# Kernel tuning notes

Hardware: AMD Instinct MI355X
Metric: run time of the kernel (lower is better)

Reference implementation:

```python
import jax, jax.numpy as jnp
import numpy as np

N = 50000          # nodes
E = 800000         # edges (avg degree 16)
NFEAT = 128        # dim_touched / gcn_nfeat
NHID = 96
NCLASS = 64
EXTRA = 32         # extra MLP-only features
NHID1, NHID2 = 128, 64
NN = 70            # top-k threshold rank
EPS = 1e-5         # BatchNorm1d eps


def setup_inputs() -> dict:
    key = jax.random.key(0)
    ks = jax.random.split(key, 24)
    x = jax.random.normal(ks[0], (N, NFEAT + EXTRA + 1), jnp.float32)
    grp = jax.random.randint(ks[1], (N,), 0, 2).astype(jnp.float32)
    x = x.at[:, -1].set(grp)  # last column is the group flag (target_group == 0)
    row = jax.random.randint(ks[2], (E,), 0, N, dtype=jnp.int32)
    col = jax.random.randint(ks[3], (E,), 0, N, dtype=jnp.int32)
    val = jax.random.uniform(ks[4], (E,), jnp.float32)

    def p(k, shape):
        return (jax.random.normal(k, shape, jnp.float32) * 0.05)

    return dict(
        x=x, row=row, col=col, val=val,
        W1=p(ks[5], (NFEAT, NHID)), b1=p(ks[6], (NHID,)),
        W2=p(ks[7], (NHID, NHID)), b2=p(ks[8], (NHID,)),
        W3=p(ks[9], (NHID, NHID)), b3=p(ks[10], (NHID,)),
        W4=p(ks[11], (NHID, NHID)), b4=p(ks[12], (NHID,)),
        W5=p(ks[13], (NHID, NCLASS)), b5=p(ks[14], (NCLASS,)),
        M1w=p(ks[15], (NCLASS + EXTRA, NHID1)), M1b=p(ks[16], (NHID1,)),
        M2w=p(ks[17], (NHID1, NHID2)), M2b=p(ks[18], (NHID2,)),
        M3w=p(ks[19], (NHID2, 1)), M3b=p(ks[20], (1,)),
    )


def _bn(h):
    # fresh BatchNorm1d in training mode, affine at default init (gamma=1, beta=0)
    m = jnp.mean(h, axis=0)
    v = jnp.mean((h - m) ** 2, axis=0)  # biased variance, as used for normalization
    return (h - m) * jax.lax.rsqrt(v + EPS)


def _gc(h, row, col, val, W, b):
    # GraphConvolution: spmm(adj, h @ W) + b, adj in COO form
    s = h @ W                                            # [N, out]
    msg = val[:, None] * s[col]                          # [E, out]
    agg = jax.ops.segment_sum(msg, row, num_segments=N)  # [N, out]
    return agg + b


def reference(x, row, col, val, W1, b1, W2, b2, W3, b3, W4, b4, W5, b5,
              M1w, M1b, M2w, M2b, M3w, M3b):
    h = x[:, :NFEAT]
    h = _bn(jax.nn.relu(_gc(h, row, col, val, W1, b1)))
    h = _bn(jax.nn.relu(_gc(h, row, col, val, W2, b2)))
    h = _bn(jax.nn.relu(_gc(h, row, col, val, W3, b3)))
    h = _bn(jax.nn.relu(_gc(h, row, col, val, W4, b4)))
    h = jax.nn.relu(_gc(h, row, col, val, W5, b5))        # [N, NCLASS]

    feat = jnp.concatenate([h, x[:, NFEAT:-1]], axis=1)   # [N, NCLASS+EXTRA]
    m = jax.nn.relu(feat @ M1w + M1b)
    m = jax.nn.relu(m @ M2w + M2b)
    m = m @ M3w + M3b                                     # [N, 1]

    # mask out target_group rows with the global min
    m = jnp.where(x[:, -1:] == 0.0, jnp.min(m), m)        # [N, 1]

    # top-70 threshold: value at descending rank NN
    thresh = jax.lax.top_k(m[:, 0], NN + 1)[0][NN]
    recip = jax.lax.stop_gradient(1.0 / m)                # torch reciprocal on detach()
    mask = jnp.where(m > thresh, recip, jnp.zeros_like(m))
    return m * mask
```

## Files before the change

kernel.cpp:

```cpp
#include <hip/hip_runtime.h>
#include <cstdint>
#include <cstddef>

#define XLD 161
#define GA  2048

typedef float f4u __attribute__((ext_vector_type(4), aligned(4)));
typedef float f4a __attribute__((ext_vector_type(4)));
typedef float f3u __attribute__((ext_vector_type(3), aligned(4)));
typedef float f2a __attribute__((ext_vector_type(2)));

__global__ void hist_kernel(const int* __restrict__ row, int* __restrict__ cnt, int E) {
    for (int e = blockIdx.x * blockDim.x + threadIdx.x; e < E; e += gridDim.x * blockDim.x)
        atomicAdd(&cnt[row[e]], 1);
}

__global__ __launch_bounds__(256)
void scan1_kernel(const int* __restrict__ cnt, int* __restrict__ offs,
                  int* __restrict__ bsums, int n) {
    int t = threadIdx.x;
    int gid = blockIdx.x * 256 + t;
    int v = (gid < n) ? cnt[gid] : 0;
    int x = v;
#pragma unroll
    for (int o = 1; o < 64; o <<= 1) { int y = __shfl_up(x, o); if ((t & 63) >= o) x += y; }
    __shared__ int ws[4];
    if ((t & 63) == 63) ws[t >> 6] = x;
    __syncthreads();
    int add = 0;
    for (int w = 0; w < (t >> 6); w++) add += ws[w];
    int incl = x + add;
    if (gid < n) offs[gid] = incl - v;
    if (t == 255) bsums[blockIdx.x] = incl;
}

__global__ __launch_bounds__(256)
void scan2_kernel(int* __restrict__ bsums, int nb) {
    int t = threadIdx.x;
    int v = (t < nb) ? bsums[t] : 0;
    int x = v;
#pragma unroll
    for (int o = 1; o < 64; o <<= 1) { int y = __shfl_up(x, o); if ((t & 63) >= o) x += y; }
    __shared__ int ws[4];
    if ((t & 63) == 63) ws[t >> 6] = x;
    __syncthreads();
    int add = 0;
    for (int w = 0; w < (t >> 6); w++) add += ws[w];
    if (t < nb) bsums[t] = x + add - v;
}

__global__ void scan3_kernel(int* __restrict__ offs, int* __restrict__ cursor,
                             const int* __restrict__ bsums, int n, int E) {
    int gid = blockIdx.x * 256 + threadIdx.x;
    if (gid < n) {
        int o = offs[gid] + bsums[blockIdx.x];
        offs[gid] = o;
        cursor[gid] = o;
    }
    if (gid == 0) offs[n] = E;
}

__global__ void scatter_kernel(const int* __restrict__ row, const int* __restrict__ col,
                               const float* __restrict__ val, int* __restrict__ cursor,
                               int2* __restrict__ cvA, int E) {
    for (int e = blockIdx.x * blockDim.x + threadIdx.x; e < E; e += gridDim.x * blockDim.x) {
        int r = row[e];
        int p = atomicAdd(&cursor[r], 1);
        cvA[p] = make_int2(col[e], __float_as_int(val[e]));
    }
}

template <int LC, bool WVS>
__global__ __launch_bounds__(256)
void aggP(const float* __restrict__ S, int ldS, const int* __restrict__ offs,
          const int2* __restrict__ cvA,
          float* __restrict__ Aout, float* __restrict__ vout, int n) {
    int lane = threadIdx.x & 63;
    int lg   = lane & 31;
    int grp  = threadIdx.x >> 5;
    int sh   = lane & 32;

    for (int node = blockIdx.x * 8 + grp; node < n; node += gridDim.x * 8) {
        int e0 = offs[node], e1 = offs[node + 1];
        float acc[LC];
#pragma unroll
        for (int a = 0; a < LC; a++) acc[a] = 0.f;
        float vsum = 0.f;

        for (int e = e0; e < e1; e += 32) {
            int   idx = e + lg;
            int2  cv = (idx < e1) ? cvA[idx] : make_int2(0, 0);
            int   ce = cv.x;
            float ve = __int_as_float(cv.y);
            int   cnt = min(32, e1 - e);
#pragma unroll 8
            for (int j = 0; j < cnt; j++) {
                int   c = __shfl(ce, sh + j);
                float v = __shfl(ve, sh + j);
                const float* srow = S + (size_t)c * ldS + LC * lg;
                if (LC == 3) {
                    f3u g = *(const f3u*)srow;
                    acc[0] = fmaf(v, g[0], acc[0]);
                    acc[1] = fmaf(v, g[1], acc[1]);
                    acc[2] = fmaf(v, g[2], acc[2]);
                } else {
                    f4u g = *(const f4u*)srow;
                    acc[0] = fmaf(v, g[0], acc[0]);
                    acc[1] = fmaf(v, g[1], acc[1]);
                    acc[2] = fmaf(v, g[2], acc[2]);
                    acc[3] = fmaf(v, g[3], acc[3]);
                }
                vsum += v;
            }
        }

        float* orow = Aout + (size_t)node * (32 * LC) + LC * lg;
        if (LC == 3) {
            f3u o; o[0] = acc[0]; o[1] = acc[1]; o[2] = acc[2];
            *(f3u*)orow = o;
        } else {
            f4u o; o[0] = acc[0]; o[1] = acc[1]; o[2] = acc[2]; o[3] = acc[3];
            *(f4u*)orow = o;
        }
        if (WVS && lg == 0) vout[node] = vsum;
    }
}

__global__ __launch_bounds__(256)
void aggB(const float* __restrict__ S, const int* __restrict__ offs,
          const int2* __restrict__ cvA, const float* __restrict__ bias,
          float* __restrict__ Hout, float* __restrict__ vout,
          float* __restrict__ pbuf, int n) {
    __shared__ float sS[96], sQ[96];
    int t = threadIdx.x;
    if (t < 96) { sS[t] = 0.f; sQ[t] = 0.f; }
    __syncthreads();
    int lane = t & 63, lg = lane & 31, grp = t >> 5, sh = lane & 32;
    float bb[3];
    bb[0] = bias[3 * lg]; bb[1] = bias[3 * lg + 1]; bb[2] = bias[3 * lg + 2];
    float ps[3] = {0.f, 0.f, 0.f}, pq[3] = {0.f, 0.f, 0.f};

    for (int node = blockIdx.x * 8 + grp; node < n; node += gridDim.x * 8) {
        int e0 = offs[node], e1 = offs[node + 1];
        float acc[3] = {0.f, 0.f, 0.f};
        float vsum = 0.f;
        for (int e = e0; e < e1; e += 32) {
            int   idx = e + lg;
            int2  cv = (idx < e1) ? cvA[idx] : make_int2(0, 0);
            int   ce = cv.x;
            float ve = __int_as_float(cv.y);
            int   cnt = min(32, e1 - e);
#pragma unroll 8
            for (int j = 0; j < cnt; j++) {
                int   c = __shfl(ce, sh + j);
                float v = __shfl(ve, sh + j);
                const float* srow = S + (size_t)c * 96 + 3 * lg;
                f3u g = *(const f3u*)srow;
                acc[0] = fmaf(v, g[0], acc[0]);
                acc[1] = fmaf(v, g[1], acc[1]);
                acc[2] = fmaf(v, g[2], acc[2]);
                vsum += v;
            }
        }
        float* orow = Hout + (size_t)node * 96 + 3 * lg;
        f3u o;
#pragma unroll
        for (int a = 0; a < 3; a++) {
            float v = fmaxf(acc[a] + bb[a], 0.f);
            o[a] = v;
            ps[a] += v; pq[a] += v * v;
        }
        *(f3u*)orow = o;
        if (lg == 0) vout[node] = vsum;
    }
#pragma unroll
    for (int a = 0; a < 3; a++) {
        atomicAdd(&sS[3 * lg + a], ps[a]);
        atomicAdd(&sQ[3 * lg + a], pq[a]);
    }
    __syncthreads();
    if (t < 96) {
        pbuf[(size_t)blockIdx.x * 192 + t]      = sS[t];
        pbuf[(size_t)blockIdx.x * 192 + 96 + t] = sQ[t];
    }
}

__global__ __launch_bounds__(256)
void bn_reduce(const float* __restrict__ pbuf, float* __restrict__ stats, int nb) {
    int t = threadIdx.x;
    if (t < 192) {
        float s = 0.f;
        for (int pb = blockIdx.x; pb < nb; pb += gridDim.x)
            s += pbuf[(size_t)pb * 192 + t];
        atomicAdd(&stats[t], s);
    }
}

__global__ __launch_bounds__(256)
void aggC(const float* __restrict__ S, const int* __restrict__ offs,
          const int2* __restrict__ cvA, const float* __restrict__ bias,
          const float* __restrict__ cb, const float* __restrict__ vsum,
          float* __restrict__ Hout, int n) {
    int lane = threadIdx.x & 63, lg = lane & 31, grp = threadIdx.x >> 5, sh = lane & 32;
    float bb0 = bias[2 * lg], bb1 = bias[2 * lg + 1];
    float cc0 = cb[2 * lg],   cc1 = cb[2 * lg + 1];

    for (int node = blockIdx.x * 8 + grp; node < n; node += gridDim.x * 8) {
        int e0 = offs[node], e1 = offs[node + 1];
        float a0 = 0.f, a1 = 0.f;
        for (int e = e0; e < e1; e += 32) {
            int   idx = e + lg;
            int2  cv = (idx < e1) ? cvA[idx] : make_int2(0, 0);
            int   ce = cv.x;
            float ve = __int_as_float(cv.y);
            int   cnt = min(32, e1 - e);
#pragma unroll 8
            for (int j = 0; j < cnt; j++) {
                int   c = __shfl(ce, sh + j);
                float v = __shfl(ve, sh + j);
                f2a g = *(const f2a*)(S + (size_t)c * 64 + 2 * lg);
                a0 = fmaf(v, g[0], a0);
                a1 = fmaf(v, g[1], a1);
            }
        }
        float vs = vsum[node];
        f2a o;
        o[0] = fmaxf(a0 + vs * cc0 + bb0, 0.f);
        o[1] = fmaxf(a1 + vs * cc1 + bb1, 0.f);
        *(f2a*)(Hout + (size_t)node * 64 + 2 * lg) = o;
    }
}

template <int CT>
__device__ inline void ldw(const float* p, float* wv) {
    if constexpr (CT == 4) { *(f4a*)wv = *(const f4a*)p; }
    else if constexpr (CT == 6) { *(f3u*)wv = *(const f3u*)p; *(f3u*)(wv + 3) = *(const f3u*)(p + 3); }
    else { *(f4a*)wv = *(const f4a*)p; *(f4a*)(wv + 4) = *(const f4a*)(p + 4); }
}

template <int K, int C, bool DOBN, bool HASCB, bool LIN = false, bool DOT = false>
__global__ __launch_bounds__(256)
void gemmF(const float* __restrict__ A1, int ld1, int split,
           const float* __restrict__ A2, int ld2,
           const float* __restrict__ W, const float* __restrict__ bias,
           const float* __restrict__ cbv, const float* __restrict__ vsum,
           float* __restrict__ Out, float* __restrict__ bsum,
           float* __restrict__ bsumsq, int n) {
    constexpr int CT = C / 16;
    __shared__ float Wc[16 * C];
    __shared__ float At[16][68];
    __shared__ float redS[DOBN ? C : 1];
    __shared__ float redQ[DOBN ? C : 1];

    int t  = threadIdx.x;
    int tc = t & 15, tr = t >> 4;
    int row0 = blockIdx.x * 64;

    if (DOBN && t < C) { redS[t] = 0.f; redQ[t] = 0.f; }

    int srow = t >> 2;
    int gr = row0 + srow; if (gr >= n) gr = n - 1;
    int kh = (t & 3) * 4;

    float acc[4][CT];
#pragma unroll
    for (int i = 0; i < 4; i++)
#pragma unroll
        for (int c = 0; c < CT; c++) acc[i][c] = 0.f;

    for (int kb = 0; kb < K; kb += 16) {
        __syncthreads();
        for (int i = t * 4; i < 16 * C; i += 1024)
            *(f4a*)&Wc[i] = *(const f4u*)&W[(size_t)kb * C + i];
        {
            int kg = kb + kh;
            const float* src = (kg < split) ? (A1 + (size_t)gr * ld1 + kg)
                                            : (A2 + (size_t)gr * ld2 + (kg - split));
            f4u v = *(const f4u*)src;
#pragma unroll
            for (int e = 0; e < 4; e++) At[kh + e][srow] = v[e];
        }
        __syncthreads();
#pragma unroll
        for (int kk = 0; kk < 16; kk++) {
            f4a av = *(const f4a*)&At[kk][tr * 4];
            float wv[CT];
            ldw<CT>(&Wc[kk * C + tc * CT], wv);
#pragma unroll
            for (int i = 0; i < 4; i++)
#pragma unroll
                for (int c = 0; c < CT; c++) acc[i][c] = fmaf(av[i], wv[c], acc[i][c]);
        }
    }

    if constexpr (DOT) {
        float bb2[CT], ww[CT];
#pragma unroll
        for (int c = 0; c < CT; c++) { bb2[c] = bias[tc * CT + c]; ww[c] = cbv[tc * CT + c]; }
        float b3 = vsum[0];
        float lmin = 3.4e38f;
#pragma unroll
        for (int i = 0; i < 4; i++) {
            float d = 0.f;
#pragma unroll
            for (int c = 0; c < CT; c++) d = fmaf(fmaxf(acc[i][c] + bb2[c], 0.f), ww[c], d);
            d += __shfl_xor(d, 1); d += __shfl_xor(d, 2);
            d += __shfl_xor(d, 4); d += __shfl_xor(d, 8);
            int r = row0 + tr * 4 + i;
            if (tc == 0 && r < n) {
                float mv = d + b3;
                Out[r] = mv;
                lmin = fminf(lmin, mv);
            }
        }
        __shared__ float smin[16];
        if (tc == 0) smin[tr] = lmin;
        __syncthreads();
        if (t == 0) {
            float mn = smin[0];
#pragma unroll
            for (int i2 = 1; i2 < 16; i2++) mn = fminf(mn, smin[i2]);
            unsigned u = __float_as_uint(mn);
            unsigned key = (u >> 31) ? ~u : (u | 0x80000000u);
            atomicMin((unsigned*)bsum, key);
        }
        return;
    }

    float bb[CT], cc[CT];
#pragma unroll
    for (int c = 0; c < CT; c++) {
        bb[c] = LIN ? 0.f : bias[tc * CT + c];
        cc[c] = HASCB ? cbv[tc * CT + c] : 0.f;
    }
    float ps[CT], pq[CT];
#pragma unroll
    for (int c = 0; c < CT; c++) { ps[c] = 0.f; pq[c] = 0.f; }

#pragma unroll
    for (int i = 0; i < 4; i++) {
        int r = row0 + tr * 4 + i;
        if (r < n) {
            float vs = HASCB ? vsum[r] : 0.f;
            float* o = Out + (size_t)r * C + tc * CT;
#pragma unroll
            for (int c = 0; c < CT; c++) {
                float v = acc[i][c] + vs * cc[c] + bb[c];
                if (!LIN) v = fmaxf(v, 0.f);
                o[c] = v;
                if (DOBN) { ps[c] += v; pq[c] += v * v; }
            }
        }
    }
    if (DOBN) {
#pragma unroll
        for (int c = 0; c < CT; c++) {
            ps[c] += __shfl_xor(ps[c], 16);
            ps[c] += __shfl_xor(ps[c], 32);
            pq[c] += __shfl_xor(pq[c], 16);
            pq[c] += __shfl_xor(pq[c], 32);
        }
        if ((t & 48) == 0) {
#pragma unroll
            for (int c = 0; c < CT; c++) {
                atomicAdd(&redS[tc * CT + c], ps[c]);
                atomicAdd(&redQ[tc * CT + c], pq[c]);
            }
        }
        __syncthreads();
        if (t < C) {
            atomicAdd(&bsum[t], redS[t]);
            atomicAdd(&bsumsq[t], redQ[t]);
        }
    }
}

template <int C>
__global__ __launch_bounds__(256)
void fold_kernel(const float* __restrict__ W, float* __restrict__ bsum,
                 float* __restrict__ bsumsq, float* __restrict__ Wf,
                 float* __restrict__ cb, int N) {
    __shared__ float mean[96], inv[96];
    int t = threadIdx.x;
    float rn = 1.0f / (float)N;
    if (t < 96) {
        float mu  = bsum[t] * rn;
        float var = bsumsq[t] * rn - mu * mu;
        mean[t] = mu;
        inv[t]  = rsqrtf(var + 1e-5f);
        bsum[t] = 0.f;
        bsumsq[t] = 0.f;
    }
    __syncthreads();
    for (int i = t; i < 96 * C; i += 256) {
        int k = i / C;
        Wf[i] = inv[k] * W[i];
    }
    if (t < C) {
        float s = 0.f;
        for (int k = 0; k < 96; k++) s += mean[k] * inv[k] * W[k * C + t];
        cb[t] = -s;
    }
}

__device__ inline unsigned fkey(float f) {
    unsigned u = __float_as_uint(f);
    return (u >> 31) ? ~u : (u | 0x80000000u);
}

__global__ __launch_bounds__(256)
void where_hist(const float* __restrict__ x, float* __restrict__ m,
                const unsigned* __restrict__ gmin, unsigned* __restrict__ h0, int n) {
    __shared__ unsigned lh[256];
    int t = threadIdx.x;
    lh[t] = 0u;
    __syncthreads();
    unsigned k = *gmin;
    unsigned u = (k >> 31) ? (k ^ 0x80000000u) : ~k;
    float g = __uint_as_float(u);
    for (int i = blockIdx.x * 256 + t; i < n; i += gridDim.x * 256) {
        float mv = m[i];
        if (x[(size_t)i * XLD + 160] == 0.0f) { mv = g; m[i] = mv; }
        atomicAdd(&lh[fkey(mv) >> 24], 1u);
    }
    __syncthreads();
    if (lh[t]) atomicAdd(&h0[t], lh[t]);
}

__global__ __launch_bounds__(256)
void sel_pick8(const unsigned* __restrict__ h, const unsigned* __restrict__ kres,
               int kconst, unsigned* __restrict__ outb, unsigned* __restrict__ outk) {
    int t = threadIdx.x;
    int bin = 255 - t;
    unsigned k = kres ? *kres : (unsigned)kconst;
    unsigned c = h[bin];
    unsigned x = c;
#pragma unroll
    for (int o = 1; o < 64; o <<= 1) { unsigned y = __shfl_up(x, o); if ((t & 63) >= o) x += y; }
    __shared__ unsigned ws[4];
    if ((t & 63) == 63) ws[t >> 6] = x;
    __syncthreads();
    unsigned add = 0;
    for (int w = 0; w < (t >> 6); w++) add += ws[w];
    unsigned incl = x + add, excl = incl - c;
    if (excl < k && k <= incl) { *outb = (unsigned)bin; *outk = k - excl; }
}

__global__ __launch_bounds__(256)
void sel_hist8b(const float* __restrict__ m, const unsigned* __restrict__ pick,
                unsigned* __restrict__ h1, int n) {
    __shared__ unsigned lh[256];
    int t = threadIdx.x;
    lh[t] = 0u;
    __syncthreads();
    unsigned b0 = pick[0];
    for (int i = blockIdx.x * 256 + t; i < n; i += gridDim.x * 256) {
        unsigned key = fkey(m[i]);
        if ((key >> 24) == b0) atomicAdd(&lh[(key >> 16) & 255u], 1u);
    }
    __syncthreads();
    if (lh[t]) atomicAdd(&h1[t], lh[t]);
}

__global__ void sel_collect(const float* __restrict__ m, const unsigned* __restrict__ pick,
                            unsigned* __restrict__ sbuf, unsigned* __restrict__ scnt, int n) {
    unsigned pfx = (pick[0] << 8) | pick[2];
    for (int i = blockIdx.x * blockDim.x + threadIdx.x; i < n; i += gridDim.x * blockDim.x) {
        unsigned key = fkey(m[i]);
        if ((key >> 16) == pfx) sbuf[atomicAdd(scnt, 1u)] = key;
    }
}

__global__ __launch_bounds__(1024)
void sel_final(const unsigned* __restrict__ sbuf, const unsigned* __restrict__ scnt,
               const unsigned* __restrict__ pick, float* __restrict__ thresh) {
    __shared__ unsigned hist[256];
    __shared__ unsigned spfx;
    __shared__ int skk;
    int t = threadIdx.x;
    int ns = (int)*scnt;
    if (t == 0) { spfx = ((pick[0] << 8) | pick[2]) << 16; skk = (int)pick[3]; }
    __syncthreads();
    for (int pass = 0; pass < 2; ++pass) {
        if (t < 256) hist[t] = 0u;
        __syncthreads();
        int shift = 8 - 8 * pass;
        unsigned pfxmask = (pass == 0) ? 0xFFFF0000u : 0xFFFFFF00u;
        unsigned pfx = spfx;
        for (int i = t; i < ns; i += 1024) {
            unsigned key = sbuf[i];
            if ((key & pfxmask) == pfx) atomicAdd(&hist[(key >> shift) & 255u], 1u);
        }
        __syncthreads();
        if (t == 0) {
            int cum = 0, kk = skk, chosen = 0;
            for (int b = 255; b >= 0; b--) {
                cum += (int)hist[b];
                if (cum >= kk) { chosen = b; kk -= (cum - (int)hist[b]); break; }
            }
            spfx = pfx | ((unsigned)chosen << shift);
            skk = kk;
        }
        __syncthreads();
    }
    if (t == 0) {
        unsigned key = spfx;
        unsigned u = (key >> 31) ? (key ^ 0x80000000u) : ~key;
        *thresh = __uint_as_float(u);
    }
}

__global__ void mask_kernel(const float* __restrict__ m, const float* __restrict__ thresh,
                            float* __restrict__ out, int n) {
    int i = blockIdx.x * blockDim.x + threadIdx.x;
    if (i < n) {
        float t = *thresh, v = m[i];
        out[i] = (v > t) ? v * (1.0f / v) : 0.0f;
    }
}

extern "C" void kernel_launch(void* const* d_in, const int* in_sizes, int n_in,
                              void* d_out, int out_size, void* d_ws, size_t ws_size,
                              hipStream_t stream) {
    const float* x   = (const float*)d_in[0];
    const int*   row = (const int*)d_in[1];
    const int*   col = (const int*)d_in[2];
    const float* val = (const float*)d_in[3];
    const float* W1  = (const float*)d_in[4];
    const float* b1  = (const float*)d_in[5];
    const float* W2  = (const float*)d_in[6];
    const float* b2  = (const float*)d_in[7];
    const float* W3  = (const float*)d_in[8];
    const float* b3  = (const float*)d_in[9];
    const float* W4  = (const float*)d_in[10];
    const float* b4  = (const float*)d_in[11];
    const float* W5  = (const float*)d_in[12];
    const float* b5  = (const float*)d_in[13];
    const float* M1w = (const float*)d_in[14];
    const float* M1b = (const float*)d_in[15];
    const float* M2w = (const float*)d_in[16];
    const float* M2b = (const float*)d_in[17];
    const float* M3w = (const float*)d_in[18];
    const float* M3b = (const float*)d_in[19];

    const int n = in_sizes[0] / XLD;
    const int E = in_sizes[1];

    char* ws = (char*)d_ws;
    size_t off = 0;
    auto carve = [&](size_t bytes) -> void* {
        void* p = ws + off;
        off = (off + bytes + 255) & ~(size_t)255;
        return p;
    };
    int*      offs   = (int*)carve((size_t)(n + 1) * 4);
    int*      cursor = (int*)carve((size_t)n * 4);
    int*      bsums  = (int*)carve(256 * 4);
    int2*     cvA    = (int2*)carve((size_t)E * 8);
    float*    hA     = (float*)carve((size_t)n * 128 * 4);
    float*    hB     = (float*)carve((size_t)n * 128 * 4);
    float*    Wf     = (float*)carve(96 * 96 * 4);
    float*    stats  = (float*)carve(192 * 4);
    float*    cb     = (float*)carve(96 * 4);
    float*    vsum   = (float*)carve((size_t)n * 4);
    float*    m      = (float*)carve((size_t)n * 4);
    unsigned* gmin   = (unsigned*)carve(4);
    float*    thresh = (float*)carve(4);
    unsigned* h0     = (unsigned*)carve(256 * 4);
    unsigned* h1     = (unsigned*)carve(256 * 4);
    unsigned* sbuf   = (unsigned*)carve((size_t)n * 4);
    unsigned* scnt   = (unsigned*)carve(4);
    unsigned* pick   = (unsigned*)carve(16);
    float*    pbuf   = (float*)carve((size_t)GA * 192 * 4);
    float* bsum   = stats;
    float* bsumsq = stats + 96;

    hipMemsetAsync(cursor, 0, (size_t)n * 4, stream);
    hipMemsetAsync(stats, 0, 192 * 4, stream);
    hipMemsetAsync(gmin, 0xFF, 4, stream);
    hipMemsetAsync(h0, 0, 256 * 4, stream);
    hipMemsetAsync(h1, 0, 256 * 4, stream);
    hipMemsetAsync(scnt, 0, 4, stream);

    const int nb = (n + 255) / 256;
    hist_kernel<<<2048, 256, 0, stream>>>(row, cursor, E);
    scan1_kernel<<<nb, 256, 0, stream>>>(cursor, offs, bsums, n);
    scan2_kernel<<<1, 256, 0, stream>>>(bsums, nb);
    scan3_kernel<<<nb, 256, 0, stream>>>(offs, cursor, bsums, n, E);
    scatter_kernel<<<2048, 256, 0, stream>>>(row, col, val, cursor, cvA, E);

    const int gB = (n + 63) / 64;

    gemmF<128, 96, false, false, true><<<gB, 256, 0, stream>>>(x, XLD, 128, x, XLD,
        W1, b1, nullptr, nullptr, hB, bsum, bsumsq, n);
    aggB<<<GA, 256, 0, stream>>>(hB, offs, cvA, b1, hA, vsum, pbuf, n);
    bn_reduce<<<64, 256, 0, stream>>>(pbuf, stats, GA);

    fold_kernel<96><<<1, 256, 0, stream>>>(W2, bsum, bsumsq, Wf, cb, n);
    aggP<3, false><<<GA, 256, 0, stream>>>(hA, 96, offs, cvA, hB, nullptr, n);
    gemmF<96, 96, true, true><<<gB, 256, 0, stream>>>(hB, 96, 96, hB, 96,
        Wf, b2, cb, vsum, hA, bsum, bsumsq, n);

    fold_kernel<96><<<1, 256, 0, stream>>>(W3, bsum, bsumsq, Wf, cb, n);
    aggP<3, false><<<GA, 256, 0, stream>>>(hA, 96, offs, cvA, hB, nullptr, n);
    gemmF<96, 96, true, true><<<gB, 256, 0, stream>>>(hB, 96, 96, hB, 96,
        Wf, b3, cb, vsum, hA, bsum, bsumsq, n);

    fold_kernel<96><<<1, 256, 0, stream>>>(W4, bsum, bsumsq, Wf, cb, n);
    aggP<3, false><<<GA, 256, 0, stream>>>(hA, 96, offs, cvA, hB, nullptr, n);
    gemmF<96, 96, true, true><<<gB, 256, 0, stream>>>(hB, 96, 96, hB, 96,
        Wf, b4, cb, vsum, hA, bsum, bsumsq, n);

    fold_kernel<64><<<1, 256, 0, stream>>>(W5, bsum, bsumsq, Wf, cb, n);
    gemmF<96, 64, false, false, true><<<gB, 256, 0, stream>>>(hA, 96, 96, hA, 96,
        Wf, b5, nullptr, nullptr, hB, bsum, bsumsq, n);
    aggC<<<GA, 256, 0, stream>>>(hB, offs, cvA, b5, cb, vsum, hA, n);

    gemmF<96, 128, false, false><<<gB, 256, 0, stream>>>(hA, 64, 64, x + 128, XLD,
        M1w, M1b, nullptr, nullptr, hB, bsum, bsumsq, n);
    gemmF<128, 64, false, false, false, true><<<gB, 256, 0, stream>>>(hB, 128, 128, hB, 128,
        M2w, M2b, M3w, M3b, m, (float*)gmin, nullptr, n);

    where_hist<<<64, 256, 0, stream>>>(x, m, gmin, h0, n);

    sel_pick8<<<1, 256, 0, stream>>>(h0, nullptr, 71, &pick[0], &pick[1]);
    sel_hist8b<<<64, 256, 0, stream>>>(m, pick, h1, n);
    sel_pick8<<<1, 256, 0, stream>>>(h1, &pick[1], 0, &pick[2], &pick[3]);
    sel_collect<<<64, 256, 0, stream>>>(m, pick, sbuf, scnt, n);
    sel_final<<<1, 1024, 0, stream>>>(sbuf, scnt, pick, thresh);

    mask_kernel<<<(n + 255) / 256, 256, 0, stream>>>(m, thresh, (float*)d_out, n);
}
```

Measured before the change: 725.0 us.

## Replace per-edge atomic CSR scatter with two-pass bucketed scatter via shared memory

Replaces the single-pass CSR build, which did one global atomic per edge on the row cursor, with a two-pass bucket sort. Pass one groups edges into 256-row buckets using shared-memory counters and one global atomic per bucket per block, writing int4 records into a temporary buffer that reuses hA. Pass two sorts each bucket's edges into final positions in shared memory and writes them out contiguously. Large buckets fall back to global atomics. This cuts global atomic contention and scattered writes, at the cost of an extra pass over a 16-byte-per-edge intermediate buffer.

```diff
diff --git a/kernel.cpp b/kernel.cpp
--- a/kernel.cpp
+++ b/kernel.cpp
@@ -4,6 +4,7 @@
 
 #define XLD 161
 #define GA  2048
+#define SBCAP 6144
 
 typedef float f4u __attribute__((ext_vector_type(4), aligned(4)));
 typedef float f4a __attribute__((ext_vector_type(4)));
@@ -50,23 +51,75 @@
 }
 
 __global__ void scan3_kernel(int* __restrict__ offs, int* __restrict__ cursor,
-                             const int* __restrict__ bsums, int n, int E) {
+                             const int* __restrict__ bsums, int* __restrict__ bcur,
+                             int n, int E) {
     int gid = blockIdx.x * 256 + threadIdx.x;
     if (gid < n) {
         int o = offs[gid] + bsums[blockIdx.x];
         offs[gid] = o;
         cursor[gid] = o;
+        if ((gid & 255) == 0) bcur[gid >> 8] = o;
     }
     if (gid == 0) offs[n] = E;
 }
 
-__global__ void scatter_kernel(const int* __restrict__ row, const int* __restrict__ col,
-                               const float* __restrict__ val, int* __restrict__ cursor,
-                               int2* __restrict__ cvA, int E) {
-    for (int e = blockIdx.x * blockDim.x + threadIdx.x; e < E; e += gridDim.x * blockDim.x) {
-        int r = row[e];
-        int p = atomicAdd(&cursor[r], 1);
-        cvA[p] = make_int2(col[e], __float_as_int(val[e]));
+__global__ __launch_bounds__(256)
+void scatterA(const int* __restrict__ row, const int* __restrict__ col,
+              const float* __restrict__ val, int* __restrict__ bcur,
+              int4* __restrict__ tmpE, int E, int nbk) {
+    __shared__ int cntL[256], baseL[256], rankL[256];
+    int t = threadIdx.x;
+    cntL[t] = 0; rankL[t] = 0;
+    __syncthreads();
+    int e0 = blockIdx.x * 2048;
+    int r[8], b[8];
+#pragma unroll
+    for (int j = 0; j < 8; j++) {
+        int e = e0 + j * 256 + t;
+        if (e < E) { r[j] = row[e]; b[j] = r[j] >> 8; atomicAdd(&cntL[b[j]], 1); }
+        else { r[j] = -1; b[j] = 0; }
+    }
+    __syncthreads();
+    if (t < nbk && cntL[t]) baseL[t] = atomicAdd(&bcur[t], cntL[t]);
+    __syncthreads();
+#pragma unroll
+    for (int j = 0; j < 8; j++) {
+        int e = e0 + j * 256 + t;
+        if (e < E) {
+            int q = atomicAdd(&rankL[b[j]], 1);
+            tmpE[baseL[b[j]] + q] = make_int4(r[j], col[e], __float_as_int(val[e]), 0);
+        }
+    }
+}
+
+__global__ __launch_bounds__(256)
+void scatterB(const int4* __restrict__ tmpE, const int* __restrict__ offs,
+              int* __restrict__ gcur, int2* __restrict__ cvA, int n) {
+    __shared__ int cur[256];
+    __shared__ int2 stage[SBCAP];
+    int b = blockIdx.x, t = threadIdx.x;
+    int rowLo = b << 8;
+    int rowHi = min(n, rowLo + 256);
+    int base = offs[rowLo];
+    int end  = offs[rowHi];
+    int len  = end - base;
+    if (rowLo + t < rowHi) cur[t] = offs[rowLo + t] - base;
+    __syncthreads();
+    if (len <= SBCAP) {
+        for (int i = t; i < len; i += 256) {
+            int4 ed = tmpE[base + i];
+            int q = atomicAdd(&cur[ed.x - rowLo], 1);
+            stage[q] = make_int2(ed.y, ed.z);
+        }
+        __syncthreads();
+        for (int i = t; i < len; i += 256)
+            cvA[base + i] = stage[i];
+    } else {
+        for (int i = t; i < len; i += 256) {
+            int4 ed = tmpE[base + i];
+            int p = atomicAdd(&gcur[ed.x], 1);
+            cvA[p] = make_int2(ed.y, ed.z);
+        }
     }
 }
 
@@ -545,6 +598,7 @@
 
     const int n = in_sizes[0] / XLD;
     const int E = in_sizes[1];
+    const int nbk = (n + 255) >> 8;
 
     char* ws = (char*)d_ws;
     size_t off = 0;
@@ -556,6 +610,7 @@
     int*      offs   = (int*)carve((size_t)(n + 1) * 4);
     int*      cursor = (int*)carve((size_t)n * 4);
     int*      bsums  = (int*)carve(256 * 4);
+    int*      bcur   = (int*)carve(256 * 4);
     int2*     cvA    = (int2*)carve((size_t)E * 8);
     float*    hA     = (float*)carve((size_t)n * 128 * 4);
     float*    hB     = (float*)carve((size_t)n * 128 * 4);
@@ -574,6 +629,7 @@
     float*    pbuf   = (float*)carve((size_t)GA * 192 * 4);
     float* bsum   = stats;
     float* bsumsq = stats + 96;
+    int4*  tmpE   = (int4*)hA;
 
     hipMemsetAsync(cursor, 0, (size_t)n * 4, stream);
     hipMemsetAsync(stats, 0, 192 * 4, stream);
@@ -586,8 +642,9 @@
     hist_kernel<<<2048, 256, 0, stream>>>(row, cursor, E);
     scan1_kernel<<<nb, 256, 0, stream>>>(cursor, offs, bsums, n);
     scan2_kernel<<<1, 256, 0, stream>>>(bsums, nb);
-    scan3_kernel<<<nb, 256, 0, stream>>>(offs, cursor, bsums, n, E);
-    scatter_kernel<<<2048, 256, 0, stream>>>(row, col, val, cursor, cvA, E);
+    scan3_kernel<<<nb, 256, 0, stream>>>(offs, cursor, bsums, bcur, n, E);
+    scatterA<<<(E + 2047) / 2048, 256, 0, stream>>>(row, col, val, bcur, tmpE, E, nbk);
+    scatterB<<<nbk, 256, 0, stream>>>(tmpE, offs, cursor, cvA, n);
 
     const int gB = (n + 63) / 64;
 
```

Measured after the change: 690.0 us. -4.8%, faster.
